# Kernel optimization log

Hardware: AMD Instinct MI355X
Metric: run time of the kernel (lower is better)

## Reference

```python
import jax, jax.numpy as jnp
import numpy as np

FOCAL_ALPHA = 0.25
FOCAL_GAMMA = 2.0
W_FOCAL = 1.0
W_DICE = 1.0
COST_MASK = 1.0
COST_DICE = 1.0
COST_CLASS = 0.0
CLS_W_MATCHED = 2.0
CLS_W_NOOBJ = 0.1


def hungarian(cost):
    """Exact Hungarian (shortest augmenting path). cost: [n, m] numpy, n <= m.
    Returns ans[i] = column assigned to row i."""
    cost = np.asarray(cost, dtype=np.float64)
    n, m = cost.shape
    assert n <= m
    INF = 1e18
    u = np.zeros(n + 1)
    v = np.zeros(m + 1)
    p = np.zeros(m + 1, dtype=np.int64)   # p[j] = row (1-indexed) matched to col j
    way = np.zeros(m + 1, dtype=np.int64)
    for i in range(1, n + 1):
        p[0] = i
        j0 = 0
        minv = np.full(m + 1, INF)
        used = np.zeros(m + 1, dtype=bool)
        while True:
            used[j0] = True
            i0 = p[j0]
            cur = cost[i0 - 1, :] - u[i0] - v[1:]
            upd = (~used[1:]) & (cur < minv[1:])
            minv[1:][upd] = cur[upd]
            way[1:][upd] = j0
            free = ~used[1:]
            j1 = int(np.argmin(np.where(free, minv[1:], INF))) + 1
            delta = minv[j1]
            u[p[used]] += delta
            v[used] -= delta
            minv[1:][free] -= delta
            j0 = j1
            if p[j0] == 0:
                break
        while j0:
            j1 = way[j0]
            p[j0] = p[j1]
            j0 = j1
    ans = np.zeros(n, dtype=np.int64)
    for j in range(1, m + 1):
        if p[j] > 0:
            ans[p[j] - 1] = j - 1
    return ans


def _focal_terms(logits):
    # sigmoid focal loss split into positive/negative per-point terms
    p = jax.nn.sigmoid(logits)
    pos = FOCAL_ALPHA * (1.0 - p) ** FOCAL_GAMMA * jax.nn.softplus(-logits)
    neg = (1.0 - FOCAL_ALPHA) * p ** FOCAL_GAMMA * jax.nn.softplus(logits)
    return pos, neg


def _inst_class_first(labels, seg, num_inst, C):
    # class of each instance = class of its FIRST point (reverse scatter so
    # earlier occurrences overwrite later ones), clamped to [0, C-1]
    inst_class = jnp.zeros((num_inst,), jnp.int32).at[labels[::-1]].set(seg[::-1])
    return jnp.clip(inst_class, 0, C - 1)


def _match_cost(pm, logits, tgt, inst_class):
    # pm [Q,N] mask logits, tgt [I,N] binary target masks
    N = pm.shape[1]
    pos, neg = _focal_terms(pm)
    c_focal = (pos @ tgt.T + neg @ (1.0 - tgt).T) / N            # [Q,I]
    p = jax.nn.sigmoid(pm)
    num = 2.0 * (p @ tgt.T)
    den = p.sum(1, keepdims=True) + tgt.sum(1)[None, :]
    c_dice = 1.0 - (num + 1.0) / (den + 1.0)                     # [Q,I]
    prob = jax.nn.softmax(logits, axis=-1)
    c_class = -prob[:, inst_class]                               # [Q,I]
    return COST_MASK * c_focal + COST_DICE * c_dice + COST_CLASS * c_class


def _batch_loss(pm, logits, labels, seg, num_inst, idx_q):
    Q, N = pm.shape
    C = logits.shape[1] - 1
    tgt = (labels[None, :] == jnp.arange(num_inst)[:, None]).astype(pm.dtype)  # [I,N]
    pm_m = pm[idx_q]                                                           # [I,N]
    # focal loss over matched (mask, target-mask) pairs
    pos, neg = _focal_terms(pm_m)
    focal = jnp.mean(pos * tgt + neg * (1.0 - tgt))
    # dice loss
    p = jax.nn.sigmoid(pm_m)
    num = 2.0 * jnp.sum(p * tgt, axis=1)
    den = jnp.sum(p, axis=1) + jnp.sum(tgt, axis=1)
    dice = jnp.mean(1.0 - (num + 1.0) / (den + 1.0))
    # classification: matched queries -> instance class, unmatched -> no-object (C)
    inst_class = _inst_class_first(labels, seg, num_inst, C)
    logp = jax.nn.log_softmax(logits, axis=-1)                 # [Q,C+1]
    ce_matched = -jnp.mean(logp[idx_q, inst_class])
    unmatched = jnp.ones((Q,), bool).at[idx_q].set(False)
    n_un = jnp.sum(unmatched)
    ce_noobj = -jnp.sum(jnp.where(unmatched, logp[:, C], 0.0)) / jnp.maximum(n_un, 1)
    cls = CLS_W_MATCHED * ce_matched + CLS_W_NOOBJ * ce_noobj
    return W_FOCAL * focal + W_DICE * dice + cls


def setup_inputs() -> dict:
    key = jax.random.key(0)
    k1, k2, k3, k4 = jax.random.split(key, 4)
    B, Q, N, I, C1 = 2, 100, 200000, 64, 6
    pred_masks = jax.random.normal(k1, (B, Q, N), dtype=jnp.float32)
    pred_logits = jax.random.normal(k2, (B, Q, C1), dtype=jnp.float32)
    labels = jax.random.randint(k3, (B, N), 0, I).astype(jnp.int32)
    # guarantee every instance id appears at least once
    labels = labels.at[:, :I].set(jnp.arange(I, dtype=jnp.int32)[None, :])
    seg = jax.random.randint(k4, (B, N), 0, C1 - 1).astype(jnp.int32)
    return {"pred_masks": pred_masks, "pred_logits": pred_logits,
            "labels": labels, "seg": seg, "num_instances": I}


def reference(pred_masks, pred_logits, labels, seg, num_instances):
    B = pred_masks.shape[0]
    C = pred_logits.shape[2] - 1
    losses = []
    for b in range(B):  # small fixed batch of events with ragged semantics
        pm, lg, lb, sg = pred_masks[b], pred_logits[b], labels[b], seg[b]
        tgt = (lb[None, :] == jnp.arange(num_instances)[:, None]).astype(pm.dtype)
        inst_class = _inst_class_first(lb, sg, num_instances, C)
        cost = _match_cost(pm, lg, tgt, inst_class)              # [Q,I]
        idx_q = jnp.asarray(hungarian(np.asarray(jax.lax.stop_gradient(cost)).T),
                            dtype=jnp.int32)                     # [I]
        losses.append(_batch_loss(pm, lg, lb, sg, num_instances, idx_q))
    return jnp.mean(jnp.stack(losses))
```

## Files before the change

kernel.cpp:

```cpp
#include <hip/hip_runtime.h>
#include <cstdint>
#include <cstddef>

constexpr int kB  = 2;
constexpr int kQ  = 100;
constexpr int kN  = 200000;
constexpr int kI  = 64;
constexpr int kC1 = 6;
constexpr int kQP = 128;
constexpr int kPB = 32;

__global__ void prep_kernel(const int* __restrict__ labels,
                            int* __restrict__ cntPart, int* __restrict__ fiPart) {
  const int b = blockIdx.y;
  const int tid = threadIdx.x;
  __shared__ int lcnt[kI], lmin[kI];
  if (tid < kI) { lcnt[tid] = 0; lmin[tid] = 0x7FFFFFFF; }
  __syncthreads();
  for (int n = blockIdx.x * blockDim.x + tid; n < kN; n += gridDim.x * blockDim.x) {
    int l = labels[(size_t)b * kN + n] & (kI - 1);
    atomicAdd(&lcnt[l], 1);
    atomicMin(&lmin[l], n);
  }
  __syncthreads();
  if (tid < kI) {
    int o = (b * kPB + blockIdx.x) * kI + tid;
    cntPart[o] = lcnt[tid];
    fiPart[o]  = lmin[tid];
  }
}

__global__ __launch_bounds__(1024) void bucket_kernel(
    const float* __restrict__ pm, const int* __restrict__ labels,
    const int* __restrict__ cntPart,
    float* __restrict__ fS, float* __restrict__ pS,
    float* __restrict__ negTot, float* __restrict__ pTot,
    float* __restrict__ costT) {
  const int q = blockIdx.x, b = blockIdx.y;
  const int tid = threadIdx.x;
  const int w = tid >> 6;
  constexpr float kScale = 16384.0f;
  constexpr double kInv  = 1.0 / 16384.0;

  __shared__ unsigned long long lS[16][kI];
  ((unsigned long long*)lS)[tid] = 0ull;
  __syncthreads();

  const float4* row4 = (const float4*)(pm + ((size_t)(b * kQ + q)) * kN);
  const int4*   lab4 = (const int4*)(labels + (size_t)b * kN);
  float negAcc = 0.f;
  constexpr int NV4 = kN / 4;

  for (int it = tid; it < NV4; it += 1024) {
    float4 xv = row4[it];
    int4   lv = lab4[it];
#define PROC(x_, l_) do {                                   \
      float x = (x_); int l = (l_) & (kI - 1);              \
      float xc = fminf(fmaxf(x, -60.f), 60.f);              \
      float t  = __expf(-xc);                               \
      float r  = 1.0f / (1.0f + t);         \
      float L  = __logf(1.0f + t);        \
      float omp = t * r;                         \
      float pos = 0.25f * omp * omp * L;                    \
      float neg = 0.75f * r * r * (L + x);                  \
      int fi = __float2int_rn((pos - neg) * kScale);        \
      int pi = __float2int_rn(r * kScale);                  \
      unsigned long long pk =                               \
        (unsigned long long)(((long long)fi) << 32) +       \
        (unsigned long long)(unsigned int)pi;               \
      atomicAdd(&lS[w][l], pk);                             \
      negAcc += neg;                                        \
    } while (0)
    PROC(xv.x, lv.x); PROC(xv.y, lv.y); PROC(xv.z, lv.z); PROC(xv.w, lv.w);
#undef PROC
  }
  __syncthreads();

  __shared__ float ffS[kI], fpS[kI];
  if (tid < kI) {
    long long fsum = 0, psum = 0;
    for (int ww = 0; ww < 16; ++ww) {
      unsigned long long s = lS[ww][tid];
      fsum += (int)(s >> 32);
      psum += (long long)(s & 0xFFFFFFFFull);
    }
    ffS[tid] = (float)((double)fsum * kInv);
    fpS[tid] = (float)((double)psum * kInv);
  }
  for (int off = 32; off; off >>= 1) negAcc += __shfl_down(negAcc, off);
  __shared__ float wsum[16];
  if ((tid & 63) == 0) wsum[w] = negAcc;
  __syncthreads();
  __shared__ float s_negTot, s_pTot;
  if (tid == 0) {
    float s = 0.f;
    for (int ww = 0; ww < 16; ++ww) s += wsum[ww];
    s_negTot = s;
  }
  if (tid < kI) {
    float vv = fpS[tid];
    for (int off = 32; off; off >>= 1) vv += __shfl_down(vv, off);
    if (tid == 0) s_pTot = vv;
  }
  __syncthreads();

  if (tid < kI) {
    int cv = 0;
    for (int blk = 0; blk < kPB; ++blk)
      cv += cntPart[(b * kPB + blk) * kI + tid];
    float f = ffS[tid], pp = fpS[tid];
    int bq = b * kQ + q;
    fS[(size_t)bq * kI + tid] = f;
    pS[(size_t)bq * kI + tid] = pp;
    float cf = (f + s_negTot) * (1.0f / kN);
    float cd = 1.0f - (2.0f * pp + 1.0f) / (s_pTot + (float)cv + 1.0f);
    costT[(size_t)(b * kI + tid) * kQ + q] = cf + cd;
    if (tid == 0) { negTot[bq] = s_negTot; pTot[bq] = s_pTot; }
  }
}

template<int CTRL>
__device__ __forceinline__ int dpp_mov(int x) {
  return __builtin_amdgcn_update_dpp(x, x, CTRL, 0xF, 0xF, false);
}
template<int CTRL>
__device__ __forceinline__ float dpp_minf(float a) {
  int o = dpp_mov<CTRL>(__float_as_int(a));
  return fminf(a, __int_as_float(o));
}
__device__ __forceinline__ double rl64(double x, int l) {
  int lo = __builtin_amdgcn_readlane(__double2loint(x), l);
  int hi = __builtin_amdgcn_readlane(__double2hiint(x), l);
  return __hiloint2double(hi, lo);
}
__device__ __forceinline__ float rlf(float x, int l) {
  return __int_as_float(__builtin_amdgcn_readlane(__float_as_int(x), l));
}
__device__ __forceinline__ float packF(float v, int cid) {
  int bb = __float_as_int(v);
  bb = (bb & ~0x7F) | cid;
  return __int_as_float(bb);
}
__device__ __forceinline__ float maskF(float v) {
  return __int_as_float(__float_as_int(v) & ~0x7F);
}
__device__ __forceinline__ void comb2f(float& m1, float& m2, float o1, float o2) {
  float lo = fminf(m1, o1);
  float hi = fmaxf(m1, o1);
  m2 = fminf(hi, fminf(m2, o2));
  m1 = lo;
}
template<int CTRL>
__device__ __forceinline__ void dpp_comb2f(float& m1, float& m2) {
  float o1 = __int_as_float(dpp_mov<CTRL>(__float_as_int(m1)));
  float o2 = __int_as_float(dpp_mov<CTRL>(__float_as_int(m2)));
  comb2f(m1, m2, o1, o2);
}

__global__ void hungarian_kernel(const float* __restrict__ costT,
                                 int* __restrict__ idx_q) {
  const int b = blockIdx.x;
  const int lane = threadIdx.x;
  __shared__ float costL[kI * kQP];
  __shared__ int claim[kQP];
  for (int t = lane; t < kI * kQP; t += 64) {
    int row = t >> 7, col = t & (kQP - 1);
    costL[t] = (col < kQ) ? costT[(size_t)b * kI * kQ + row * kQ + col] : 1e30f;
  }
  claim[lane] = 127;
  claim[lane + 64] = 127;
  __syncthreads();

  const int col0 = 2 * lane, col1 = 2 * lane + 1;
  double v0 = 0.0, v1 = 0.0;
  int p0 = 0, p1 = 0;

  double m = 1e18; int jm = 0;
  {
    const float4* r4 = (const float4*)&costL[lane * kQP];
    for (int k4 = 0; k4 < kQ / 4; ++k4) {
      float4 c = r4[k4];
      int k = 4 * k4;
      if ((double)c.x < m) { m = (double)c.x; jm = k; }
      if ((double)c.y < m) { m = (double)c.y; jm = k + 1; }
      if ((double)c.z < m) { m = (double)c.z; jm = k + 2; }
      if ((double)c.w < m) { m = (double)c.w; jm = k + 3; }
    }
  }
  double u_r = m;

  atomicMin(&claim[jm], lane);
  __syncthreads();
  unsigned long long rowM = __ballot(claim[jm] == lane);
  {
    int w0 = claim[col0], w1 = claim[col1];
    p0 = (w0 < 64) ? w0 + 1 : 0;
    p1 = (w1 < 64) ? w1 + 1 : 0;
  }

  unsigned long long pool = ~rowM;
  unsigned long long leftover = 0ull;
  for (int pass = 0; pass < 2; ++pass) {
    unsigned long long next = 0ull;
    unsigned long long cur = pool;
    while (cur) {
      int i = __builtin_ctzll(cur) + 1;
      cur &= cur - 1;
      float2 cc = *(const float2*)&costL[(i - 1) * kQP + col0];
      double e0 = (double)cc.x - v0;
      double e1 = (double)cc.y - v1;
      float pf0 = packF((float)e0, col0);
      float pf1 = packF((float)e1, col1);
      float m1 = fminf(pf0, pf1), m2 = fmaxf(pf0, pf1);
      dpp_comb2f<0xB1>(m1, m2);
      dpp_comb2f<0x4E>(m1, m2);
      dpp_comb2f<0x141>(m1, m2);
      dpp_comb2f<0x140>(m1, m2);
      float a1 = rlf(m1, 0),  a2 = rlf(m2, 0);
      { float b1 = rlf(m1, 16), b2 = rlf(m2, 16); comb2f(a1, a2, b1, b2); }
      { float b1 = rlf(m1, 32), b2 = rlf(m2, 32); comb2f(a1, a2, b1, b2); }
      { float b1 = rlf(m1, 48), b2 = rlf(m2, 48); comb2f(a1, a2, b1, b2); }
      int cid1 = __builtin_amdgcn_readfirstlane(__float_as_int(a1) & 0x7F);
      int cid2 = __builtin_amdgcn_readfirstlane(__float_as_int(a2) & 0x7F);
      int L1 = cid1 >> 1; bool sW = cid1 & 1;
      int L2 = cid2 >> 1; bool sW2 = cid2 & 1;
      double min1 = sW  ? rl64(e1, L1) : rl64(e0, L1);
      double min2 = sW2 ? rl64(e1, L2) : rl64(e0, L2);
      double dv = min2 - min1;
      u_r = (lane == i - 1) ? min2 : u_r;
      int i0 = sW ? __builtin_amdgcn_readlane(p1, L1)
                  : __builtin_amdgcn_readlane(p0, L1);
      bool mine0 = (!sW) && (lane == L1);
      bool mine1 = sW && (lane == L1);
      p0 = mine0 ? i : p0;  v0 -= mine0 ? dv : 0.0;
      p1 = mine1 ? i : p1;  v1 -= mine1 ? dv : 0.0;
      if (i0 != 0) {
        if (pass == 0) next |= 1ull << (i0 - 1);
        else           leftover |= 1ull << (i0 - 1);
      }
    }
    pool = next;
  }
  leftover |= pool;

  const float SENT = packF(1e30f, 127);
  float u_f  = (float)u_r;
  float v0f  = (float)v0;
  float v1f  = (float)v1;
  for (int i = 1; i <= kI; ++i) {
    if (!((leftover >> (i - 1)) & 1ull)) continue;
    float minv0 = SENT, minv1 = SENT;
    int way0 = 0, way1 = 0;
    bool used0 = false, used1 = false;
    bool onpath = (lane == i - 1);
    int j0 = 0, j1 = 0;
    float2 cc = *(const float2*)&costL[(i - 1) * kQP + col0];
    float c0 = cc.x, c1 = cc.y;
    float ui0 = rlf(u_f, i - 1);
    for (int guard = 0; guard < 2 * kQ; ++guard) {
      float pk0 = packF(c0 - ui0 - v0f, col0);
      bool up0 = (!used0) && (pk0 < minv0);
      minv0 = up0 ? pk0 : minv0;
      way0  = up0 ? j0 : way0;
      float pk1 = packF(c1 - ui0 - v1f, col1);
      bool up1 = (!used1) && (pk1 < minv1);
      minv1 = up1 ? pk1 : minv1;
      way1  = up1 ? j0 : way1;
      float bm = fminf(minv0, minv1);
      bm = dpp_minf<0xB1>(bm);
      bm = dpp_minf<0x4E>(bm);
      bm = dpp_minf<0x141>(bm);
      bm = dpp_minf<0x140>(bm);
      float g = fminf(fminf(rlf(bm, 0), rlf(bm, 16)),
                      fminf(rlf(bm, 32), rlf(bm, 48)));
      int gi = __builtin_amdgcn_readfirstlane(__float_as_int(g));
      int cid = gi & 0x7F;
      float delta = __int_as_float(gi & ~0x7F);
      const int  L = cid >> 1;
      const bool s = cid & 1;
      int r1 = s ? __builtin_amdgcn_readlane(p1, L)
                 : __builtin_amdgcn_readlane(p0, L);
      int i0n = (r1 > 0) ? r1 : 1;
      float2 cn = *(const float2*)&costL[(i0n - 1) * kQP + col0];

      u_f += onpath ? delta : 0.f;
      v0f -= used0 ? delta : 0.f;
      v1f -= used1 ? delta : 0.f;
      minv0 = used0 ? minv0 : packF(maskF(minv0) - delta, col0);
      minv1 = used1 ? minv1 : packF(maskF(minv1) - delta, col1);
      bool w0 = (!s) && (lane == L);
      bool w1 = s && (lane == L);
      used0 = used0 || w0;
      used1 = used1 || w1;
      minv0 = w0 ? SENT : minv0;
      minv1 = w1 ? SENT : minv1;
      j1 = cid + 1;

      if (r1 == 0) break;
      onpath = onpath || (lane == r1 - 1);
      ui0 = rlf(u_f, r1 - 1);
      j0 = j1;
      c0 = cn.x;
      c1 = cn.y;
    }
    int jc = j1;
    while (jc) {
      int Lc = (jc - 1) >> 1, sc = (jc - 1) & 1;
      int jw = sc ? __builtin_amdgcn_readlane(way1, Lc)
                  : __builtin_amdgcn_readlane(way0, Lc);
      int pw;
      if (jw == 0) pw = i;
      else {
        int Lw = (jw - 1) >> 1, sw = (jw - 1) & 1;
        pw = sw ? __builtin_amdgcn_readlane(p1, Lw)
                : __builtin_amdgcn_readlane(p0, Lw);
      }
      bool w0 = (!sc) && (lane == Lc);
      bool w1 = sc && (lane == Lc);
      p0 = w0 ? pw : p0;
      p1 = w1 ? pw : p1;
      jc = jw;
    }
  }
  if (col0 < kQ && p0 > 0) idx_q[b * kI + (p0 - 1)] = col0;
  if (col1 < kQ && p1 > 0) idx_q[b * kI + (p1 - 1)] = col1;
}

__device__ __forceinline__ float reduce128(float v, float* scratch, int tid) {
  for (int off = 32; off; off >>= 1) v += __shfl_down(v, off);
  __syncthreads();
  if ((tid & 63) == 0) scratch[tid >> 6] = v;
  __syncthreads();
  return scratch[0] + scratch[1];
}

__global__ void loss_kernel(const float* __restrict__ logits, const int* __restrict__ seg,
                            const float* __restrict__ fS, const float* __restrict__ pS,
                            const float* __restrict__ negTot, const float* __restrict__ pTot,
                            const int* __restrict__ cntPart, const int* __restrict__ fiPart,
                            const int* __restrict__ idx_q, float* __restrict__ out) {
  const int tid = threadIdx.x;
  __shared__ float lse[kQ];
  __shared__ int matched[kQ];
  __shared__ float scratch[2];
  float total = 0.f;
  for (int b = 0; b < kB; ++b) {
    if (tid < kQ) {
      const float* lr = logits + (size_t)(b * kQ + tid) * kC1;
      float m = lr[0];
#pragma unroll
      for (int c = 1; c < kC1; ++c) m = fmaxf(m, lr[c]);
      float s = 0.f;
#pragma unroll
      for (int c = 0; c < kC1; ++c) s += __expf(lr[c] - m);
      lse[tid] = m + __logf(s);
      matched[tid] = 0;
    }
    __syncthreads();
    if (tid < kI) matched[idx_q[b * kI + tid]] = 1;
    __syncthreads();

    float fo = 0.f, di = 0.f, cm = 0.f, no = 0.f, nu = 0.f;
    if (tid < kI) {
      int cv = 0, fi = 0x7FFFFFFF;
      for (int blk = 0; blk < kPB; ++blk) {
        int o = (b * kPB + blk) * kI + tid;
        cv += cntPart[o];
        fi = min(fi, fiPart[o]);
      }
      int qi = idx_q[b * kI + tid];
      int bq = b * kQ + qi;
      float f = fS[(size_t)bq * kI + tid];
      fo = f + negTot[bq];
      float pp = pS[(size_t)bq * kI + tid];
      di = 1.f - (2.f * pp + 1.f) / (pTot[bq] + (float)cv + 1.f);
      fi = fi < kN ? fi : kN - 1;
      int ci = seg[(size_t)b * kN + fi];
      ci = ci < 0 ? 0 : (ci > kC1 - 2 ? kC1 - 2 : ci);
      cm = logits[(size_t)bq * kC1 + ci] - lse[qi];
    }
    if (tid < kQ && !matched[tid]) {
      no = logits[(size_t)(b * kQ + tid) * kC1 + (kC1 - 1)] - lse[tid];
      nu = 1.f;
    }
    float foS = reduce128(fo, scratch, tid);
    float diS = reduce128(di, scratch, tid);
    float cmS = reduce128(cm, scratch, tid);
    float noS = reduce128(no, scratch, tid);
    float nuS = reduce128(nu, scratch, tid);

    float focal = foS / ((float)kI * (float)kN);
    float dice  = diS / (float)kI;
    float cem   = -cmS / (float)kI;
    float cen   = -noS / fmaxf(nuS, 1.f);
    total += focal + dice + 2.0f * cem + 0.1f * cen;
    __syncthreads();
  }
  if (tid == 0) out[0] = total * (1.0f / kB);
}

extern "C" void kernel_launch(void* const* d_in, const int* in_sizes, int n_in,
                              void* d_out, int out_size, void* d_ws, size_t ws_size,
                              hipStream_t stream) {
  const float* pm     = (const float*)d_in[0];
  const float* logits = (const float*)d_in[1];
  const int*   labels = (const int*)d_in[2];
  const int*   seg    = (const int*)d_in[3];

  char* w = (char*)d_ws;
  float* fS       = (float*)w; w += (size_t)kB * kQ * kI * 4;
  float* pS       = (float*)w; w += (size_t)kB * kQ * kI * 4;
  float* negTot   = (float*)w; w += (size_t)kB * kQ * 4;
  float* pTot     = (float*)w; w += (size_t)kB * kQ * 4;
  float* costT    = (float*)w; w += (size_t)kB * kI * kQ * 4;
  int*   cntPart  = (int*)w;   w += (size_t)kB * kPB * kI * 4;
  int*   fiPart   = (int*)w;   w += (size_t)kB * kPB * kI * 4;
  int*   idx_q    = (int*)w;   w += (size_t)kB * kI * 4;

  prep_kernel<<<dim3(kPB, kB), 256, 0, stream>>>(labels, cntPart, fiPart);
  bucket_kernel<<<dim3(kQ, kB), 1024, 0, stream>>>(pm, labels, cntPart, fS, pS,
                                                   negTot, pTot, costT);
  hungarian_kernel<<<kB, 64, 0, stream>>>(costT, idx_q);
  loss_kernel<<<1, 128, 0, stream>>>(logits, seg, fS, pS, negTot, pTot,
                                     cntPart, fiPart, idx_q, (float*)d_out);
}
```

Baseline: 355.7 us.

## Use float in auction prepass, DPP row-broadcast reductions, finer LDS histogram split

Widens the per-wave LDS accumulation in the bucket kernel from 16 to 32 copies (one per half-wave), which is meant to reduce atomic contention on shared-memory bins. In the Hungarian kernel's initial assignment passes, double-precision potentials and 64-bit readlanes are replaced with float arithmetic. The wave-wide min reductions use DPP row_bcast15/31 steps, finishing with a single readlane of lane 63 instead of four readlanes and a readfirstlane. Float potentials may change tie-breaking or matching accuracy, and the min values are now recovered from packed floats whose low mantissa bits are masked off.

Result: slower. 367.2 us (+3.2%).

```diff
diff --git a/kernel.cpp b/kernel.cpp
--- a/kernel.cpp
+++ b/kernel.cpp
@@ -38,12 +38,13 @@
     float* __restrict__ costT) {
   const int q = blockIdx.x, b = blockIdx.y;
   const int tid = threadIdx.x;
-  const int w = tid >> 6;
+  const int w = tid >> 5;
   constexpr float kScale = 16384.0f;
   constexpr double kInv  = 1.0 / 16384.0;
 
-  __shared__ unsigned long long lS[16][kI];
-  ((unsigned long long*)lS)[tid] = 0ull;
+  __shared__ unsigned long long lS[32][kI];
+  for (int t = tid; t < 32 * kI; t += 1024)
+    ((unsigned long long*)lS)[t] = 0ull;
   __syncthreads();
 
   const float4* row4 = (const float4*)(pm + ((size_t)(b * kQ + q)) * kN);
@@ -79,7 +80,7 @@
   __shared__ float ffS[kI], fpS[kI];
   if (tid < kI) {
     long long fsum = 0, psum = 0;
-    for (int ww = 0; ww < 16; ++ww) {
+    for (int ww = 0; ww < 32; ++ww) {
       unsigned long long s = lS[ww][tid];
       fsum += (int)(s >> 32);
       psum += (long long)(s & 0xFFFFFFFFull);
@@ -89,7 +90,7 @@
   }
   for (int off = 32; off; off >>= 1) negAcc += __shfl_down(negAcc, off);
   __shared__ float wsum[16];
-  if ((tid & 63) == 0) wsum[w] = negAcc;
+  if ((tid & 63) == 0) wsum[tid >> 6] = negAcc;
   __syncthreads();
   __shared__ float s_negTot, s_pTot;
   if (tid == 0) {
@@ -128,11 +129,6 @@
   int o = dpp_mov<CTRL>(__float_as_int(a));
   return fminf(a, __int_as_float(o));
 }
-__device__ __forceinline__ double rl64(double x, int l) {
-  int lo = __builtin_amdgcn_readlane(__double2loint(x), l);
-  int hi = __builtin_amdgcn_readlane(__double2hiint(x), l);
-  return __hiloint2double(hi, lo);
-}
 __device__ __forceinline__ float rlf(float x, int l) {
   return __int_as_float(__builtin_amdgcn_readlane(__float_as_int(x), l));
 }
@@ -172,22 +168,22 @@
   __syncthreads();
 
   const int col0 = 2 * lane, col1 = 2 * lane + 1;
-  double v0 = 0.0, v1 = 0.0;
+  float v0f = 0.f, v1f = 0.f;
   int p0 = 0, p1 = 0;
 
-  double m = 1e18; int jm = 0;
+  float m = 1e30f; int jm = 0;
   {
     const float4* r4 = (const float4*)&costL[lane * kQP];
     for (int k4 = 0; k4 < kQ / 4; ++k4) {
       float4 c = r4[k4];
       int k = 4 * k4;
-      if ((double)c.x < m) { m = (double)c.x; jm = k; }
-      if ((double)c.y < m) { m = (double)c.y; jm = k + 1; }
-      if ((double)c.z < m) { m = (double)c.z; jm = k + 2; }
-      if ((double)c.w < m) { m = (double)c.w; jm = k + 3; }
-    }
-  }
-  double u_r = m;
+      if (c.x < m) { m = c.x; jm = k; }
+      if (c.y < m) { m = c.y; jm = k + 1; }
+      if (c.z < m) { m = c.z; jm = k + 2; }
+      if (c.w < m) { m = c.w; jm = k + 3; }
+    }
+  }
+  float u_f = m;
 
   atomicMin(&claim[jm], lane);
   __syncthreads();
@@ -207,33 +203,29 @@
       int i = __builtin_ctzll(cur) + 1;
       cur &= cur - 1;
       float2 cc = *(const float2*)&costL[(i - 1) * kQP + col0];
-      double e0 = (double)cc.x - v0;
-      double e1 = (double)cc.y - v1;
-      float pf0 = packF((float)e0, col0);
-      float pf1 = packF((float)e1, col1);
+      float pf0 = packF(cc.x - v0f, col0);
+      float pf1 = packF(cc.y - v1f, col1);
       float m1 = fminf(pf0, pf1), m2 = fmaxf(pf0, pf1);
       dpp_comb2f<0xB1>(m1, m2);
       dpp_comb2f<0x4E>(m1, m2);
       dpp_comb2f<0x141>(m1, m2);
       dpp_comb2f<0x140>(m1, m2);
-      float a1 = rlf(m1, 0),  a2 = rlf(m2, 0);
-      { float b1 = rlf(m1, 16), b2 = rlf(m2, 16); comb2f(a1, a2, b1, b2); }
-      { float b1 = rlf(m1, 32), b2 = rlf(m2, 32); comb2f(a1, a2, b1, b2); }
-      { float b1 = rlf(m1, 48), b2 = rlf(m2, 48); comb2f(a1, a2, b1, b2); }
-      int cid1 = __builtin_amdgcn_readfirstlane(__float_as_int(a1) & 0x7F);
-      int cid2 = __builtin_amdgcn_readfirstlane(__float_as_int(a2) & 0x7F);
+      dpp_comb2f<0x142>(m1, m2);
+      dpp_comb2f<0x143>(m1, m2);
+      float a1 = rlf(m1, 63), a2 = rlf(m2, 63);
+      int gi1 = __float_as_int(a1);
+      int cid1 = gi1 & 0x7F;
+      float min1 = __int_as_float(gi1 & ~0x7F);
+      float min2 = maskF(a2);
+      float dv = min2 - min1;
       int L1 = cid1 >> 1; bool sW = cid1 & 1;
-      int L2 = cid2 >> 1; bool sW2 = cid2 & 1;
-      double min1 = sW  ? rl64(e1, L1) : rl64(e0, L1);
-      double min2 = sW2 ? rl64(e1, L2) : rl64(e0, L2);
-      double dv = min2 - min1;
-      u_r = (lane == i - 1) ? min2 : u_r;
+      u_f = (lane == i - 1) ? min2 : u_f;
       int i0 = sW ? __builtin_amdgcn_readlane(p1, L1)
                   : __builtin_amdgcn_readlane(p0, L1);
       bool mine0 = (!sW) && (lane == L1);
       bool mine1 = sW && (lane == L1);
-      p0 = mine0 ? i : p0;  v0 -= mine0 ? dv : 0.0;
-      p1 = mine1 ? i : p1;  v1 -= mine1 ? dv : 0.0;
+      p0 = mine0 ? i : p0;  v0f -= mine0 ? dv : 0.f;
+      p1 = mine1 ? i : p1;  v1f -= mine1 ? dv : 0.f;
       if (i0 != 0) {
         if (pass == 0) next |= 1ull << (i0 - 1);
         else           leftover |= 1ull << (i0 - 1);
@@ -244,9 +236,6 @@
   leftover |= pool;
 
   const float SENT = packF(1e30f, 127);
-  float u_f  = (float)u_r;
-  float v0f  = (float)v0;
-  float v1f  = (float)v1;
   for (int i = 1; i <= kI; ++i) {
     if (!((leftover >> (i - 1)) & 1ull)) continue;
     float minv0 = SENT, minv1 = SENT;
@@ -271,9 +260,10 @@
       bm = dpp_minf<0x4E>(bm);
       bm = dpp_minf<0x141>(bm);
       bm = dpp_minf<0x140>(bm);
-      float g = fminf(fminf(rlf(bm, 0), rlf(bm, 16)),
-                      fminf(rlf(bm, 32), rlf(bm, 48)));
-      int gi = __builtin_amdgcn_readfirstlane(__float_as_int(g));
+      bm = dpp_minf<0x142>(bm);
+      bm = dpp_minf<0x143>(bm);
+      float g = rlf(bm, 63);
+      int gi = __float_as_int(g);
       int cid = gi & 0x7F;
       float delta = __int_as_float(gi & ~0x7F);
       const int  L = cid >> 1;
```
